# Kernel optimization log

Measured on AMD Instinct MI355X. Metric: run time of the kernel, lower is better.

## Reference

```python
import jax, jax.numpy as jnp
import numpy as np

D_MODEL = 1024
N_EXPERTS = 8
TOP_K = 2
LN_EPS = 1e-5


def setup_inputs() -> dict:
    key = jax.random.key(0)
    ks = jax.random.split(key, 8)
    B, S, d, E = 2, 2048, D_MODEL, N_EXPERTS
    f = 2 * d
    s_in = 0.02
    return {
        "x": jax.random.normal(ks[0], (B, S, d), jnp.float32),
        "Wg": jax.random.normal(ks[1], (d, E), jnp.float32) * s_in,
        "bg": jnp.zeros((E,), jnp.float32),
        "W1": jax.random.normal(ks[2], (E, d, f), jnp.float32) * s_in,
        "b1": jnp.zeros((E, f), jnp.float32),
        "W2": jax.random.normal(ks[3], (E, f, d), jnp.float32) * s_in,
        "b2": jnp.zeros((E, d), jnp.float32),
        "gamma": jnp.ones((d,), jnp.float32),
        "beta": jnp.zeros((d,), jnp.float32),
    }


def reference(x, Wg, bg, W1, b1, W2, b2, gamma, beta):
    # Gating + top-k routing (softmax over the selected top-k logits only)
    logits = jnp.einsum("bsd,de->bse", x, Wg) + bg            # [B,S,E]
    topk_vals, topk_idx = jax.lax.top_k(logits, TOP_K)         # [B,S,K]
    topk_w = jax.nn.softmax(topk_vals, axis=-1)                # [B,S,K]

    # Expert MLPs evaluated densely for all experts (dropout is identity in eval)
    h = jax.nn.relu(jnp.einsum("bsd,edf->bsef", x, W1) + b1)   # [B,S,E,2d]
    eo = jnp.einsum("bsef,efd->bsed", h, W2) + b2              # [B,S,E,d]

    # Gather the top-k experts' outputs per token and combine with gate weights
    sel = jnp.take_along_axis(eo, topk_idx[..., None], axis=2)  # [B,S,K,d]
    mixed = jnp.sum(sel * topk_w[..., None], axis=2)            # [B,S,d]

    # Residual + LayerNorm
    y = mixed + x
    mu = jnp.mean(y, axis=-1, keepdims=True)
    var = jnp.mean(jnp.square(y - mu), axis=-1, keepdims=True)
    return gamma * (y - mu) * jax.lax.rsqrt(var + LN_EPS) + beta
```

## Files before the change

kernel.cpp:

```cpp
#include <hip/hip_runtime.h>


typedef unsigned short ushort_t;
typedef short short8 __attribute__((ext_vector_type(8)));
typedef float f32x4 __attribute__((ext_vector_type(4)));

#define T_TOKENS 4096
#define DMODEL 1024
#define FFN 2048
#define NEXP 8
#define ECAP 1152
#define MAXSLOTS 9216
#define MT1 9
#define CNT_STRIDE 16
#define GATE_BLKS 256

__device__ __forceinline__ ushort_t f2bf(float f) {
    unsigned u = __float_as_uint(f);
    return (ushort_t)((u + 0x7fffu + ((u >> 16) & 1u)) >> 16);
}
__device__ __forceinline__ float bflo(unsigned packed) {
    return __uint_as_float(packed << 16);
}
__device__ __forceinline__ float bfhi(unsigned packed) {
    return __uint_as_float(packed & 0xffff0000u);
}

__device__ __forceinline__ void gload_lds16(const void* g, void* l) {
    __builtin_amdgcn_global_load_lds(
        (const __attribute__((address_space(1))) unsigned int*)g,
        (__attribute__((address_space(3))) unsigned int*)l,
        16, 0, 0);
}

__global__ __launch_bounds__(256) void prep_kernel(
    const float* __restrict__ W1, ushort_t* __restrict__ W1T,
    const float* __restrict__ W2, ushort_t* __restrict__ W2T,
    const float* __restrict__ x, const float* __restrict__ Wg,
    const float* __restrict__ bg,
    int* __restrict__ gcnt, int* __restrict__ slot_of,
    float* __restrict__ top_w, ushort_t* __restrict__ Xg)
{
    __shared__ __align__(16) ushort_t smem[32 * 516];
    const int b = blockIdx.x;
    const int tid = threadIdx.x;

    if (b >= GATE_BLKS) {
        int b2 = b - GATE_BLKS;
        const float* s; ushort_t* d; int N, kc, ns;
        if (b2 < 1024) {
            int e = b2 >> 7, idx = b2 & 127;
            kc = idx >> 2; ns = idx & 3;
            s = W1 + (size_t)e * DMODEL * FFN;
            d = W1T + (size_t)e * DMODEL * FFN;
            N = FFN;
        } else {
            b2 -= 1024;
            int e = b2 >> 7, idx = b2 & 127;
            kc = idx >> 1; ns = idx & 1;
            s = W2 + (size_t)e * DMODEL * FFN;
            d = W2T + (size_t)e * DMODEL * FFN;
            N = DMODEL;
        }
        const int k0 = kc * 32, n0 = ns * 512;
        ushort_t* lt = smem;
        #pragma unroll
        for (int i = 0; i < 16; i++) {
            int k = i * 2 + (tid >> 7);
            int n = (tid & 127) * 4;
            float4 v = *(const float4*)&s[(size_t)(k0 + k) * N + n0 + n];
            uint2 pk;
            pk.x = (unsigned)f2bf(v.x) | ((unsigned)f2bf(v.y) << 16);
            pk.y = (unsigned)f2bf(v.z) | ((unsigned)f2bf(v.w) << 16);
            *(uint2*)&lt[k * 516 + n] = pk;
        }
        __syncthreads();
        const int sub = tid & 3;
        const int nl0 = tid >> 2;
        #pragma unroll
        for (int it = 0; it < 8; it++) {
            int n = nl0 + it * 64;
            uint4 o;
            o.x = (unsigned)lt[(sub * 8 + 0) * 516 + n] | ((unsigned)lt[(sub * 8 + 1) * 516 + n] << 16);
            o.y = (unsigned)lt[(sub * 8 + 2) * 516 + n] | ((unsigned)lt[(sub * 8 + 3) * 516 + n] << 16);
            o.z = (unsigned)lt[(sub * 8 + 4) * 516 + n] | ((unsigned)lt[(sub * 8 + 5) * 516 + n] << 16);
            o.w = (unsigned)lt[(sub * 8 + 6) * 516 + n] | ((unsigned)lt[(sub * 8 + 7) * 516 + n] << 16);
            *(uint4*)&d[((size_t)kc * N + n0 + n) * 32 + sub * 8] = o;
        }
        return;
    }

    int* sh    = (int*)smem;
    int* hist  = sh;
    int* sbase = sh + 8;
    int* tokinf = sh + 16;
    const int lane = tid & 63, w = tid >> 6;
    if (tid < NEXP) hist[tid] = 0;
    __syncthreads();

    #pragma unroll 1
    for (int it = 0; it < 4; it++) {
        const int t = b * 16 + w * 4 + it;
        const float* xr = x + (size_t)t * DMODEL;
        float acc[8] = {0.f,0.f,0.f,0.f,0.f,0.f,0.f,0.f};
        #pragma unroll
        for (int i = 0; i < 16; i++) {
            float xv = xr[i * 64 + lane];
            const float4* wp = (const float4*)&Wg[(i * 64 + lane) * 8];
            float4 a = wp[0], bb = wp[1];
            acc[0] += xv * a.x;  acc[1] += xv * a.y;
            acc[2] += xv * a.z;  acc[3] += xv * a.w;
            acc[4] += xv * bb.x; acc[5] += xv * bb.y;
            acc[6] += xv * bb.z; acc[7] += xv * bb.w;
        }
        #pragma unroll
        for (int off = 32; off > 0; off >>= 1) {
            #pragma unroll
            for (int e = 0; e < 8; e++) acc[e] += __shfl_down(acc[e], off);
        }
        if (lane == 0) {
            float l[8];
            #pragma unroll
            for (int e = 0; e < 8; e++) l[e] = acc[e] + bg[e];
            int i0 = 0; float v0 = l[0];
            #pragma unroll
            for (int e = 1; e < 8; e++) if (l[e] > v0) { v0 = l[e]; i0 = e; }
            int i1 = -1; float v1 = -1e30f;
            #pragma unroll
            for (int e = 0; e < 8; e++) if (e != i0 && l[e] > v1) { v1 = l[e]; i1 = e; }
            float eg = expf(v1 - v0);
            float den = 1.f + eg;
            top_w[2 * t]     = 1.f / den;
            top_w[2 * t + 1] = eg / den;
            int p0 = atomicAdd(&hist[i0], 1);
            int p1 = atomicAdd(&hist[i1], 1);
            tokinf[(w * 4 + it) * 2 + 0] = i0 | (p0 << 4);
            tokinf[(w * 4 + it) * 2 + 1] = i1 | (p1 << 4);
        }
    }
    __syncthreads();
    if (tid < NEXP) sbase[tid] = atomicAdd(&gcnt[tid * CNT_STRIDE], hist[tid]);
    __syncthreads();

    #pragma unroll 1
    for (int it = 0; it < 4; it++) {
        const int t = b * 16 + w * 4 + it;
        int v0 = tokinf[(w * 4 + it) * 2 + 0];
        int v1 = tokinf[(w * 4 + it) * 2 + 1];
        int e0 = v0 & 15, e1 = v1 & 15;
        int s0 = e0 * ECAP + sbase[e0] + (v0 >> 4);
        int s1 = e1 * ECAP + sbase[e1] + (v1 >> 4);
        if (lane == 0) {
            slot_of[2 * t]     = s0;
            slot_of[2 * t + 1] = s1;
        }
        const float* xr = x + (size_t)t * DMODEL;
        #pragma unroll
        for (int j = 0; j < 4; j++) {
            int f = lane + j * 64;
            float4 xv = ((const float4*)xr)[f];
            uint2 pk;
            pk.x = (unsigned)f2bf(xv.x) | ((unsigned)f2bf(xv.y) << 16);
            pk.y = (unsigned)f2bf(xv.z) | ((unsigned)f2bf(xv.w) << 16);
            ((uint2*)(Xg + (size_t)s0 * DMODEL))[f] = pk;
            ((uint2*)(Xg + (size_t)s1 * DMODEL))[f] = pk;
        }
    }
}

template <int K, int N, bool RELU>
__global__ __launch_bounds__(256) void expert_gemm(
    const ushort_t* __restrict__ A,
    const ushort_t* __restrict__ Bt,
    const float* __restrict__ bias,
    ushort_t* __restrict__ Cout,
    const int* __restrict__ gcnt)
{
    const int e  = blockIdx.x;
    const int nt = blockIdx.y;
    const int mt = blockIdx.z;
    const int off_e = e * ECAP;
    if (mt * 128 >= gcnt[e * CNT_STRIDE]) return;

    __shared__ __align__(16) ushort_t As[128 * 32];
    __shared__ __align__(16) ushort_t Bs[128 * 32];

    const int tid  = threadIdx.x;
    const int lane = tid & 63;
    const int w    = tid >> 6;
    const int quad = lane >> 4;
    const int r16  = lane & 15;
    const int lrow = lane >> 2;
    const int lk   = (((lane & 3) ^ ((lane >> 3) & 3))) * 8;

    const size_t arow0 = (size_t)(off_e + mt * 128);
    const ushort_t* aS0 = A + (arow0 + (size_t)(2 * w + 0) * 16 + lrow) * K + lk;
    const ushort_t* aS1 = A + (arow0 + (size_t)(2 * w + 1) * 16 + lrow) * K + lk;
    const ushort_t* Bte = Bt + (size_t)e * N * K;
    const ushort_t* bS0 = Bte + (size_t)(nt * 128 + (2 * w + 0) * 16 + lrow) * 32 + lk;
    const ushort_t* bS1 = Bte + (size_t)(nt * 128 + (2 * w + 1) * 16 + lrow) * 32 + lk;
    ushort_t* aD0 = &As[(2 * w + 0) * 512];
    ushort_t* aD1 = &As[(2 * w + 1) * 512];
    ushort_t* bD0 = &Bs[(2 * w + 0) * 512];
    ushort_t* bD1 = &Bs[(2 * w + 1) * 512];

    const int wm = (w >> 1) * 64;
    const int wn = (w & 1) * 64;
    const int sw = ((r16 >> 1) & 3) ^ quad;

    f32x4 acc[4][4];
    #pragma unroll
    for (int i = 0; i < 4; i++)
        #pragma unroll
        for (int j = 0; j < 4; j++)
            acc[i][j] = (f32x4){0.f, 0.f, 0.f, 0.f};

    for (int k0 = 0; k0 < K; k0 += 32) {
        gload_lds16(aS0 + k0, aD0);
        gload_lds16(aS1 + k0, aD1);
        gload_lds16(bS0 + (size_t)k0 * N, bD0);
        gload_lds16(bS1 + (size_t)k0 * N, bD1);
        __syncthreads();
        short8 af[4], bfr[4];
        #pragma unroll
        for (int i = 0; i < 4; i++)
            af[i] = *(const short8*)&As[(wm + i * 16 + r16) * 32 + sw * 8];
        #pragma unroll
        for (int j = 0; j < 4; j++)
            bfr[j] = *(const short8*)&Bs[(wn + j * 16 + r16) * 32 + sw * 8];
        #pragma unroll
        for (int i = 0; i < 4; i++)
            #pragma unroll
            for (int j = 0; j < 4; j++)
                acc[i][j] = __builtin_amdgcn_mfma_f32_16x16x32_bf16(
                    af[i], bfr[j], acc[i][j], 0, 0, 0);
        __syncthreads();
    }

    const float* be = bias + (size_t)e * N;
    #pragma unroll
    for (int i = 0; i < 4; i++) {
        #pragma unroll
        for (int j = 0; j < 4; j++) {
            int n = nt * 128 + wn + j * 16 + r16;
            float bv = be[n];
            #pragma unroll
            for (int r = 0; r < 4; r++) {
                int m = mt * 128 + wm + i * 16 + quad * 4 + r;
                float v = acc[i][j][r] + bv;
                if (RELU) v = v > 0.f ? v : 0.f;
                Cout[(size_t)(off_e + m) * N + n] = f2bf(v);
            }
        }
    }
}

__global__ __launch_bounds__(256) void ln_kernel(
    const float* __restrict__ x, const ushort_t* __restrict__ O,
    const int* __restrict__ slot_of, const float* __restrict__ top_w,
    const float* __restrict__ gamma, const float* __restrict__ beta,
    float* __restrict__ out)
{
    int t = blockIdx.x, tid = threadIdx.x;
    int s0 = slot_of[2 * t], s1 = slot_of[2 * t + 1];
    float w0 = top_w[2 * t], w1 = top_w[2 * t + 1];
    float4 xv = ((const float4*)(x + (size_t)t * DMODEL))[tid];
    uint2 a = ((const uint2*)(O + (size_t)s0 * DMODEL))[tid];
    uint2 b = ((const uint2*)(O + (size_t)s1 * DMODEL))[tid];

    float y[4];
    y[0] = xv.x + w0 * bflo(a.x) + w1 * bflo(b.x);
    y[1] = xv.y + w0 * bfhi(a.x) + w1 * bfhi(b.x);
    y[2] = xv.z + w0 * bflo(a.y) + w1 * bflo(b.y);
    y[3] = xv.w + w0 * bfhi(a.y) + w1 * bfhi(b.y);

    float s = y[0] + y[1] + y[2] + y[3];
    float sq = y[0]*y[0] + y[1]*y[1] + y[2]*y[2] + y[3]*y[3];
    __shared__ float red[2][4];
    #pragma unroll
    for (int off = 32; off > 0; off >>= 1) {
        s += __shfl_down(s, off);
        sq += __shfl_down(sq, off);
    }
    int lane = tid & 63, wv = tid >> 6;
    if (lane == 0) { red[0][wv] = s; red[1][wv] = sq; }
    __syncthreads();
    if (tid == 0) {
        float S = red[0][0] + red[0][1] + red[0][2] + red[0][3];
        float SQ = red[1][0] + red[1][1] + red[1][2] + red[1][3];
        float mu = S * (1.f / DMODEL);
        float var = SQ * (1.f / DMODEL) - mu * mu;
        red[0][0] = mu;
        red[1][0] = rsqrtf(var + 1e-5f);
    }
    __syncthreads();
    float mu = red[0][0], inv = red[1][0];
    float4 gv = ((const float4*)gamma)[tid];
    float4 bv = ((const float4*)beta)[tid];
    float4 ov;
    ov.x = gv.x * (y[0] - mu) * inv + bv.x;
    ov.y = gv.y * (y[1] - mu) * inv + bv.y;
    ov.z = gv.z * (y[2] - mu) * inv + bv.z;
    ov.w = gv.w * (y[3] - mu) * inv + bv.w;
    ((float4*)(out + (size_t)t * DMODEL))[tid] = ov;
}

extern "C" void kernel_launch(void* const* d_in, const int* in_sizes, int n_in,
                              void* d_out, int out_size, void* d_ws, size_t ws_size,
                              hipStream_t stream)
{
    const float* x     = (const float*)d_in[0];
    const float* Wg    = (const float*)d_in[1];
    const float* bg    = (const float*)d_in[2];
    const float* W1    = (const float*)d_in[3];
    const float* b1    = (const float*)d_in[4];
    const float* W2    = (const float*)d_in[5];
    const float* b2    = (const float*)d_in[6];
    const float* gamma = (const float*)d_in[7];
    const float* beta  = (const float*)d_in[8];
    float* out = (float*)d_out;

    char* ws = (char*)d_ws;
    size_t o = 0;
    auto alloc = [&](size_t bytes) {
        size_t r = o;
        o = (o + bytes + 255) & ~(size_t)255;
        return r;
    };
    size_t o_cnt     = alloc(NEXP * CNT_STRIDE * 4);
    size_t o_topw    = alloc((size_t)T_TOKENS * 2 * 4);
    size_t o_slotof  = alloc((size_t)T_TOKENS * 2 * 4);
    size_t o_w1t     = alloc((size_t)NEXP * DMODEL * FFN * 2);
    size_t o_w2t     = alloc((size_t)NEXP * DMODEL * FFN * 2);
    size_t o_xg      = alloc((size_t)MAXSLOTS * DMODEL * 2);
    size_t o_h       = alloc((size_t)MAXSLOTS * FFN * 2);
    size_t o_obuf    = alloc((size_t)MAXSLOTS * DMODEL * 2);
    (void)ws_size; (void)in_sizes; (void)n_in; (void)out_size;

    int*      gcnt     = (int*)(ws + o_cnt);
    float*    top_w    = (float*)(ws + o_topw);
    int*      slot_of  = (int*)(ws + o_slotof);
    ushort_t* W1T      = (ushort_t*)(ws + o_w1t);
    ushort_t* W2T      = (ushort_t*)(ws + o_w2t);
    ushort_t* Xg       = (ushort_t*)(ws + o_xg);
    ushort_t* H        = (ushort_t*)(ws + o_h);
    ushort_t* Obuf     = (ushort_t*)(ws + o_obuf);

    hipMemsetAsync(gcnt, 0, NEXP * CNT_STRIDE * sizeof(int), stream);
    prep_kernel<<<GATE_BLKS + 2048, 256, 0, stream>>>(
        W1, W1T, W2, W2T, x, Wg, bg, gcnt, slot_of, top_w, Xg);
    expert_gemm<DMODEL, FFN, true>
        <<<dim3(NEXP, FFN / 128, MT1), 256, 0, stream>>>(Xg, W1T, b1, H, gcnt);
    expert_gemm<FFN, DMODEL, false>
        <<<dim3(NEXP, DMODEL / 128, MT1), 256, 0, stream>>>(H, W2T, b2, Obuf, gcnt);
    ln_kernel<<<T_TOKENS, 256, 0, stream>>>(x, Obuf, slot_of, top_w, gamma, beta, out);
}
```

Measured before the change: 302.5 us.

## Overlap W2 transpose/bf16 conversion with first expert GEMM in one launch

Moves the W2 fp32-to-bf16 transpose blocks out of the prep kernel and interleaves them inside the first expert GEMM grid. A flattened 1-D grid uses groups of 17 blocks, 9 GEMM tiles followed by 8 transpose tiles. The aim is to hide the memory-bound W2 conversion behind the compute-bound GEMM1 and shorten the prep kernel. In exchange the shared-memory size grows for GEMM1 blocks, which may lower occupancy, and the bandwidth-heavy transpose may slow the concurrent GEMM.

```diff
diff --git a/kernel.cpp b/kernel.cpp
--- a/kernel.cpp
+++ b/kernel.cpp
@@ -33,9 +33,38 @@
         16, 0, 0);
 }
 
+__device__ __forceinline__ void wt_block512(
+    const float* __restrict__ s, ushort_t* __restrict__ d,
+    int N, int kc, int n0, ushort_t* lt, int tid)
+{
+    const int k0 = kc * 32;
+    #pragma unroll
+    for (int i = 0; i < 16; i++) {
+        int k = i * 2 + (tid >> 7);
+        int n = (tid & 127) * 4;
+        float4 v = *(const float4*)&s[(size_t)(k0 + k) * N + n0 + n];
+        uint2 pk;
+        pk.x = (unsigned)f2bf(v.x) | ((unsigned)f2bf(v.y) << 16);
+        pk.y = (unsigned)f2bf(v.z) | ((unsigned)f2bf(v.w) << 16);
+        *(uint2*)&lt[k * 516 + n] = pk;
+    }
+    __syncthreads();
+    const int sub = tid & 3;
+    const int nl0 = tid >> 2;
+    #pragma unroll
+    for (int it = 0; it < 8; it++) {
+        int n = nl0 + it * 64;
+        uint4 o;
+        o.x = (unsigned)lt[(sub * 8 + 0) * 516 + n] | ((unsigned)lt[(sub * 8 + 1) * 516 + n] << 16);
+        o.y = (unsigned)lt[(sub * 8 + 2) * 516 + n] | ((unsigned)lt[(sub * 8 + 3) * 516 + n] << 16);
+        o.z = (unsigned)lt[(sub * 8 + 4) * 516 + n] | ((unsigned)lt[(sub * 8 + 5) * 516 + n] << 16);
+        o.w = (unsigned)lt[(sub * 8 + 6) * 516 + n] | ((unsigned)lt[(sub * 8 + 7) * 516 + n] << 16);
+        *(uint4*)&d[((size_t)kc * N + n0 + n) * 32 + sub * 8] = o;
+    }
+}
+
 __global__ __launch_bounds__(256) void prep_kernel(
     const float* __restrict__ W1, ushort_t* __restrict__ W1T,
-    const float* __restrict__ W2, ushort_t* __restrict__ W2T,
     const float* __restrict__ x, const float* __restrict__ Wg,
     const float* __restrict__ bg,
     int* __restrict__ gcnt, int* __restrict__ slot_of,
@@ -47,46 +76,10 @@
 
     if (b >= GATE_BLKS) {
         int b2 = b - GATE_BLKS;
-        const float* s; ushort_t* d; int N, kc, ns;
-        if (b2 < 1024) {
-            int e = b2 >> 7, idx = b2 & 127;
-            kc = idx >> 2; ns = idx & 3;
-            s = W1 + (size_t)e * DMODEL * FFN;
-            d = W1T + (size_t)e * DMODEL * FFN;
-            N = FFN;
-        } else {
-            b2 -= 1024;
-            int e = b2 >> 7, idx = b2 & 127;
-            kc = idx >> 1; ns = idx & 1;
-            s = W2 + (size_t)e * DMODEL * FFN;
-            d = W2T + (size_t)e * DMODEL * FFN;
-            N = DMODEL;
-        }
-        const int k0 = kc * 32, n0 = ns * 512;
-        ushort_t* lt = smem;
-        #pragma unroll
-        for (int i = 0; i < 16; i++) {
-            int k = i * 2 + (tid >> 7);
-            int n = (tid & 127) * 4;
-            float4 v = *(const float4*)&s[(size_t)(k0 + k) * N + n0 + n];
-            uint2 pk;
-            pk.x = (unsigned)f2bf(v.x) | ((unsigned)f2bf(v.y) << 16);
-            pk.y = (unsigned)f2bf(v.z) | ((unsigned)f2bf(v.w) << 16);
-            *(uint2*)&lt[k * 516 + n] = pk;
-        }
-        __syncthreads();
-        const int sub = tid & 3;
-        const int nl0 = tid >> 2;
-        #pragma unroll
-        for (int it = 0; it < 8; it++) {
-            int n = nl0 + it * 64;
-            uint4 o;
-            o.x = (unsigned)lt[(sub * 8 + 0) * 516 + n] | ((unsigned)lt[(sub * 8 + 1) * 516 + n] << 16);
-            o.y = (unsigned)lt[(sub * 8 + 2) * 516 + n] | ((unsigned)lt[(sub * 8 + 3) * 516 + n] << 16);
-            o.z = (unsigned)lt[(sub * 8 + 4) * 516 + n] | ((unsigned)lt[(sub * 8 + 5) * 516 + n] << 16);
-            o.w = (unsigned)lt[(sub * 8 + 6) * 516 + n] | ((unsigned)lt[(sub * 8 + 7) * 516 + n] << 16);
-            *(uint4*)&d[((size_t)kc * N + n0 + n) * 32 + sub * 8] = o;
-        }
+        int e = b2 >> 7, idx = b2 & 127;
+        wt_block512(W1 + (size_t)e * DMODEL * FFN,
+                    W1T + (size_t)e * DMODEL * FFN,
+                    FFN, idx >> 2, (idx & 3) * 512, smem, tid);
         return;
     }
 
@@ -168,24 +161,41 @@
     }
 }
 
-template <int K, int N, bool RELU>
+template <int K, int N, bool RELU, bool FUSET>
 __global__ __launch_bounds__(256) void expert_gemm(
     const ushort_t* __restrict__ A,
     const ushort_t* __restrict__ Bt,
     const float* __restrict__ bias,
     ushort_t* __restrict__ Cout,
-    const int* __restrict__ gcnt)
-{
-    const int e  = blockIdx.x;
-    const int nt = blockIdx.y;
-    const int mt = blockIdx.z;
+    const int* __restrict__ gcnt,
+    const float* __restrict__ Wsrc,
+    ushort_t* __restrict__ Wdst)
+{
+    __shared__ __align__(16) ushort_t smem[FUSET ? 32 * 516 : 8192];
+    const int tid = threadIdx.x;
+    int e, nt, mt;
+    if (FUSET) {
+        const int bid = blockIdx.x;
+        const int grp = bid / 17, rem = bid % 17;
+        if (rem >= 9) {
+            int ti = grp * 8 + (rem - 9);
+            int te = ti >> 7, idx = ti & 127;
+            wt_block512(Wsrc + (size_t)te * DMODEL * FFN,
+                        Wdst + (size_t)te * DMODEL * FFN,
+                        DMODEL, idx >> 1, (idx & 1) * 512, smem, tid);
+            return;
+        }
+        int gi = grp * 9 + rem;
+        e = gi & 7; nt = (gi >> 3) & 15; mt = gi >> 7;
+    } else {
+        e = blockIdx.x; nt = blockIdx.y; mt = blockIdx.z;
+    }
     const int off_e = e * ECAP;
     if (mt * 128 >= gcnt[e * CNT_STRIDE]) return;
 
-    __shared__ __align__(16) ushort_t As[128 * 32];
-    __shared__ __align__(16) ushort_t Bs[128 * 32];
-
-    const int tid  = threadIdx.x;
+    ushort_t* As = smem;
+    ushort_t* Bs = smem + 4096;
+
     const int lane = tid & 63;
     const int w    = tid >> 6;
     const int quad = lane >> 4;
@@ -347,11 +357,12 @@
     ushort_t* Obuf     = (ushort_t*)(ws + o_obuf);
 
     hipMemsetAsync(gcnt, 0, NEXP * CNT_STRIDE * sizeof(int), stream);
-    prep_kernel<<<GATE_BLKS + 2048, 256, 0, stream>>>(
-        W1, W1T, W2, W2T, x, Wg, bg, gcnt, slot_of, top_w, Xg);
-    expert_gemm<DMODEL, FFN, true>
-        <<<dim3(NEXP, FFN / 128, MT1), 256, 0, stream>>>(Xg, W1T, b1, H, gcnt);
-    expert_gemm<FFN, DMODEL, false>
-        <<<dim3(NEXP, DMODEL / 128, MT1), 256, 0, stream>>>(H, W2T, b2, Obuf, gcnt);
+    prep_kernel<<<GATE_BLKS + 1024, 256, 0, stream>>>(
+        W1, W1T, x, Wg, bg, gcnt, slot_of, top_w, Xg);
+    expert_gemm<DMODEL, FFN, true, true>
+        <<<2176, 256, 0, stream>>>(Xg, W1T, b1, H, gcnt, W2, W2T);
+    expert_gemm<FFN, DMODEL, false, false>
+        <<<dim3(NEXP, DMODEL / 128, MT1), 256, 0, stream>>>(
+            H, W2T, b2, Obuf, gcnt, nullptr, nullptr);
     ln_kernel<<<T_TOKENS, 256, 0, stream>>>(x, Obuf, slot_of, top_w, gamma, beta, out);
 }
```

Measured after the change: 294.6 us. 2.6% less time.
